# Optimization experiments

Hardware: AMD Instinct MI355X
Metric: run time of the kernel (lower is better)

## Reference

```python
import jax, jax.numpy as jnp
import numpy as np

B, T, H, D = 256, 128, 256, 256
N_SUB = 2  # fixed-step RK4 substeps per observation interval (replaces adaptive odeint)


def setup_inputs() -> dict:
    key = jax.random.key(0)
    ks = jax.random.split(key, 16)
    # timestamps: strictly increasing, shared across batch (torch code uses b[0,:,0])
    times = jnp.cumsum(jax.random.uniform(ks[0], (T,), minval=0.05, maxval=0.15)) + 0.1
    vals = jax.random.uniform(ks[1], (B, T))
    b = jnp.stack([jnp.broadcast_to(times, (B, T)), vals], axis=-1)  # (B,T,2)
    u = jax.random.uniform(ks[2], (B, T))
    train_m = (u < 0.4).astype(jnp.float32)
    test_m = ((u >= 0.4) & (u < 0.7)).astype(jnp.float32)
    m = train_m + test_m  # disjoint -> in {0,1}
    h0 = jnp.zeros((B, H), jnp.float32)
    s = 0.05
    p = lambda k, shp: jax.random.normal(k, shp, jnp.float32) * s
    return {
        'b': b, 'm': m, 'train_m': train_m, 'test_m': test_m, 'h0': h0,
        # ODE func: Linear(H->D) then Linear(D->H) then tanh
        'W1': p(ks[3], (D, H)), 'b1': p(ks[4], (D,)),
        'W2': p(ks[5], (H, D)), 'b2': p(ks[6], (H,)),
        # GRUCell(input_size=1, hidden=H), torch layout (3H, in)
        'W_ih': p(ks[7], (3 * H, 1)), 'W_hh': p(ks[8], (3 * H, H)),
        'b_ih': p(ks[9], (3 * H,)), 'b_hh': p(ks[10], (3 * H,)),
        # output heads: Linear(H->D), Linear(D->1), tanh
        'Wo1': p(ks[11], (D, H)), 'bo1': p(ks[12], (D,)),
        'Wo2': p(ks[13], (1, D)), 'bo2': p(ks[14], (1,)),
    }


def _gru(x, h, W_ih, W_hh, b_ih, b_hh):
    gi = x @ W_ih.T + b_ih          # (B, 3H)
    gh = h @ W_hh.T + b_hh          # (B, 3H)
    i_r, i_z, i_n = jnp.split(gi, 3, axis=-1)
    h_r, h_z, h_n = jnp.split(gh, 3, axis=-1)
    r = jax.nn.sigmoid(i_r + h_r)
    z = jax.nn.sigmoid(i_z + h_z)
    n = jnp.tanh(i_n + r * h_n)
    return (1.0 - z) * n + z * h


def _ode_rnn(b, m, train_m, test_m, h0, W1, b1, W2, b2,
             W_ih, W_hh, b_ih, b_hh, Wo1, bo1, Wo2, bo2):
    f = lambda x: jnp.tanh((x @ W1.T + b1) @ W2.T + b2)  # autonomous ODE func

    def rk4(h, t0, t1):
        dt = (t1 - t0) / N_SUB
        def sub(h, _):
            k1 = f(h)
            k2 = f(h + 0.5 * dt * k1)
            k3 = f(h + 0.5 * dt * k2)
            k4 = f(h + dt * k3)
            return h + (dt / 6.0) * (k1 + 2.0 * k2 + 2.0 * k3 + k4), None
        h, _ = jax.lax.scan(sub, h, None, length=N_SUB)
        return h

    times = b[0, :, 0]                                      # (T,)
    t0s = jnp.concatenate([jnp.zeros((1,), times.dtype), times[:-1]])
    vals = b[:, :, 1]                                       # (B,T)

    def step(h, inp):
        t0, t1, bv, mv, trm, tem = inp
        hp = rk4(h, t0, t1)                                 # (B,H)
        out = jnp.tanh((hp @ Wo1.T + bo1) @ Wo2.T + bo2)[:, 0]  # (B,)
        htrain = _gru((bv * trm)[:, None], hp, W_ih, W_hh, b_ih, b_hh)
        htest = _gru((out * tem)[:, None], hp, W_ih, W_hh, b_ih, b_hh)
        h_new = trm[:, None] * htrain + tem[:, None] * htest + (1.0 - mv)[:, None] * hp
        return h_new, out

    xs = (t0s, times, vals.T, m.T, train_m.T, test_m.T)
    _, outs = jax.lax.scan(step, h0, xs)                    # outs: (T,B)
    return outs.T                                           # (B,T)


def reference(b, m, train_m, test_m, h0, W1, b1, W2, b2,
              W_ih, W_hh, b_ih, b_hh, Wo1, bo1, Wo2, bo2):
    return _ode_rnn(b, m, train_m, test_m, h0, W1, b1, W2, b2,
                    W_ih, W_hh, b_ih, b_hh, Wo1, bo1, Wo2, bo2)
```

## Files before the change

kernel.cpp:

```cpp
#include <hip/hip_runtime.h>

#define H 256
#define T_STEPS 128
#define B_BATCH 256
#define I_LDS 48
#define XGRP 36

#define LOG2E 1.4426950408889634f

__device__ __forceinline__ float fexp2_(float x) {
#if __has_builtin(__builtin_amdgcn_exp2f)
    return __builtin_amdgcn_exp2f(x);
#else
    return exp2f(x);
#endif
}
__device__ __forceinline__ float frcp_(float x) {
#if __has_builtin(__builtin_amdgcn_rcpf)
    float r = __builtin_amdgcn_rcpf(x);
    return r * (2.0f - x * r);
#else
    return 1.0f / x;
#endif
}
__device__ __forceinline__ float tanhf_(float x) {
    float xc = fminf(fmaxf(x, -16.f), 16.f);
    float t  = fexp2_(xc * (2.f * LOG2E));
    return (t - 1.f) * frcp_(t + 1.f);
}
__device__ __forceinline__ float sigmoidf_(float x) {
    float xc = fminf(fmaxf(x, -30.f), 30.f);
    return frcp_(1.f + fexp2_(-xc * LOG2E));
}


__global__ void prep_weff(const float* __restrict__ W1, const float* __restrict__ W2,
                          const float* __restrict__ b1, const float* __restrict__ b2,
                          float* __restrict__ Weff, float* __restrict__ beff) {
    int i = blockIdx.x, j = threadIdx.x;
    const float* w2row = W2 + j * H;
    float acc = 0.f;
    for (int d = 0; d < H; ++d) acc += W1[d * H + i] * w2row[d];
    Weff[i * H + j] = acc;
    if (i == 0) {
        float bacc = b2[j];
        for (int d = 0; d < H; ++d) bacc += b1[d] * w2row[d];
        beff[j] = bacc;
    }
}

__global__ void prep_whht(const float* __restrict__ Whh, float* __restrict__ WhhT) {
    int idx = blockIdx.x * blockDim.x + threadIdx.x;
    int i = idx / 768;
    int r = idx - i * 768;
    WhhT[idx] = Whh[r * H + i];
}

__global__ void prep_wo(const float* __restrict__ Wo1, const float* __restrict__ Wo2,
                        const float* __restrict__ bo1, const float* __restrict__ bo2,
                        float* __restrict__ wo, float* __restrict__ bo) {
    int i = threadIdx.x;
    float acc = 0.f;
    for (int d = 0; d < H; ++d) acc += Wo1[d * H + i] * Wo2[d];
    wo[i] = acc;
    float p = bo1[i] * Wo2[i];
    __shared__ float red[4];
    for (int off = 32; off > 0; off >>= 1) p += __shfl_down(p, off);
    if ((i & 63) == 0) red[i >> 6] = p;
    __syncthreads();
    if (i == 0) bo[0] = red[0] + red[1] + red[2] + red[3] + bo2[0];
}


__global__ __attribute__((amdgpu_flat_work_group_size(1024, 1024),
                          amdgpu_waves_per_eu(4, 4)))
void ode_rnn_main(
    const float* __restrict__ b_in, const float* __restrict__ m_in,
    const float* __restrict__ trm_in, const float* __restrict__ tem_in,
    const float* __restrict__ h0,
    const float* __restrict__ Weff, const float* __restrict__ beff,
    const float* __restrict__ WhhT,
    const float* __restrict__ W_ih, const float* __restrict__ b_ih,
    const float* __restrict__ b_hh,
    const float* __restrict__ wo, const float* __restrict__ bo_p,
    float* __restrict__ out)
{
    const int tid = threadIdx.x;
    const int bb  = blockIdx.x;
    const int jp  = tid >> 3;
    const int e   = tid & 7;
    const int c   = e & 1;
    const int jc  = 2 * jp + c;

    __shared__ float whh_lds[I_LDS * 768];
    __shared__ __align__(16) float xsb[2][8 * XGRP];
    __shared__ __align__(16) float xsf[H];
    __shared__ float gh_lds[768];
    __shared__ float red[4];
    __shared__ float times_s[T_STEPS];
    __shared__ float bv_s[T_STEPS], trm_s[T_STEPS], tem_s[T_STEPS], m_s[T_STEPS];

    float2 wregv[32];
    #pragma unroll
    for (int il = 0; il < 32; ++il)
        wregv[il] = *(const float2*)&Weff[(32 * e + il) * H + 2 * jp];
    #pragma unroll
    for (int il = 0; il < 32; ++il)
        asm volatile("" : "+v"(wregv[il].x), "+v"(wregv[il].y));

    for (int k = tid; k < I_LDS * 768; k += 1024) whh_lds[k] = WhhT[k];
    if (tid < T_STEPS) {
        times_s[tid] = b_in[2 * tid];
        int bt = bb * T_STEPS + tid;
        bv_s[tid]  = b_in[2 * bt + 1];
        trm_s[tid] = trm_in[bt];
        tem_s[tid] = tem_in[bt];
        m_s[tid]   = m_in[bt];
    }

    float h = h0[bb * H + jc];
    const float be   = beff[jc];
    const float bihr = b_ih[jc], bihz = b_ih[H + jc], bihn = b_ih[2 * H + jc];
    const float bhhr = b_hh[jc], bhhz = b_hh[H + jc], bhhn = b_hh[2 * H + jc];
    const float wihr = W_ih[jc], wihz = W_ih[H + jc], wihn = W_ih[2 * H + jc];
    const float bo   = bo_p[0];
    const float wo_t = (tid >= 768) ? wo[tid - 768] : 0.f;

    const int pubpos = (jc >> 5) * XGRP + (jc & 31);

    if (e < 2) xsb[0][pubpos] = h;
    __syncthreads();

    #define EVAL(KOUT_) do {                                       \
        const float* xp_ = &xsb[cur][e * XGRP];                    \
        float a0_ = 0.f, a1_ = 0.f, b0_ = 0.f, b1_ = 0.f;          \
        _Pragma("unroll")                                          \
        for (int g_ = 0; g_ < 8; ++g_) {                           \
            float4 x_ = ((const float4*)xp_)[g_];                  \
            a0_ = fmaf(x_.x, wregv[4 * g_ + 0].x, a0_);            \
            b0_ = fmaf(x_.x, wregv[4 * g_ + 0].y, b0_);            \
            a1_ = fmaf(x_.y, wregv[4 * g_ + 1].x, a1_);            \
            b1_ = fmaf(x_.y, wregv[4 * g_ + 1].y, b1_);            \
            a0_ = fmaf(x_.z, wregv[4 * g_ + 2].x, a0_);            \
            b0_ = fmaf(x_.z, wregv[4 * g_ + 2].y, b0_);            \
            a1_ = fmaf(x_.w, wregv[4 * g_ + 3].x, a1_);            \
            b1_ = fmaf(x_.w, wregv[4 * g_ + 3].y, b1_);            \
        }                                                          \
        float s0_ = a0_ + a1_, s1_ = b0_ + b1_;                    \
        float v_ = (c == 0) ? s0_ : s1_;                           \
        float u_ = (c == 0) ? s1_ : s0_;                           \
        v_ += __shfl_xor(u_, 1);                                   \
        v_ += __shfl_xor(v_, 2);                                   \
        v_ += __shfl_xor(v_, 4);                                   \
        KOUT_ = tanhf_(be + v_);                                   \
    } while (0)

    #define PUBLISH(V_) do {                                       \
        if (e < 2) xsb[cur ^ 1][pubpos] = (V_);                    \
        __syncthreads();                                           \
        cur ^= 1;                                                  \
    } while (0)

    float tprev = 0.f;
    #pragma unroll 1
    for (int t = 0; t < T_STEPS; ++t) {
        float t1 = times_s[t];
        float dt = (t1 - tprev) * 0.5f;
        tprev = t1;

        int cur = 0;
        float k1, k2, k3, k4;
        #pragma unroll 1
        for (int s = 0; s < 2; ++s) {
            EVAL(k1); PUBLISH(fmaf(0.5f * dt, k1, h));
            EVAL(k2); PUBLISH(fmaf(0.5f * dt, k2, h));
            EVAL(k3); PUBLISH(fmaf(dt, k3, h));
            EVAL(k4);
            h = fmaf(dt * (1.f / 6.f), k1 + 2.f * (k2 + k3) + k4, h);
            if (s == 0) PUBLISH(h);
        }

        if (e < 2) xsf[jc] = h;
        __syncthreads();

        if (tid < 768) {
            float g0 = 0.f, g1 = 0.f, g2 = 0.f, g3 = 0.f;
            const float* wl = whh_lds + tid;
            #pragma unroll 4
            for (int i = 0; i < I_LDS; i += 4) {
                float4 xv = *(const float4*)(xsf + i);
                g0 = fmaf(xv.x, wl[(i + 0) * 768], g0);
                g1 = fmaf(xv.y, wl[(i + 1) * 768], g1);
                g2 = fmaf(xv.z, wl[(i + 2) * 768], g2);
                g3 = fmaf(xv.w, wl[(i + 3) * 768], g3);
            }
            const float* wr = WhhT + I_LDS * 768 + tid;
            #pragma unroll 8
            for (int i = 0; i < H - I_LDS; i += 4) {
                float4 xv = *(const float4*)(xsf + I_LDS + i);
                g0 = fmaf(xv.x, wr[(i + 0) * 768], g0);
                g1 = fmaf(xv.y, wr[(i + 1) * 768], g1);
                g2 = fmaf(xv.z, wr[(i + 2) * 768], g2);
                g3 = fmaf(xv.w, wr[(i + 3) * 768], g3);
            }
            gh_lds[tid] = (g0 + g1) + (g2 + g3);
        } else {
            float p = xsf[tid - 768] * wo_t;
            #pragma unroll
            for (int off = 32; off > 0; off >>= 1) p += __shfl_down(p, off);
            if ((tid & 63) == 0) red[(tid - 768) >> 6] = p;
        }
        __syncthreads();

        {
            float outv = tanhf_(red[0] + red[1] + red[2] + red[3] + bo);
            float bv = bv_s[t], trm = trm_s[t], tem = tem_s[t], mv = m_s[t];
            float ghr = gh_lds[jc] + bhhr;
            float ghz = gh_lds[256 + jc] + bhhz;
            float ghn = gh_lds[512 + jc] + bhhn;
            float x1v = bv * trm, x2v = outv * tem;

            float r1 = sigmoidf_(fmaf(x1v, wihr, bihr) + ghr);
            float z1 = sigmoidf_(fmaf(x1v, wihz, bihz) + ghz);
            float n1 = tanhf_(fmaf(x1v, wihn, bihn) + r1 * ghn);
            float h1 = (1.f - z1) * n1 + z1 * h;

            float r2 = sigmoidf_(fmaf(x2v, wihr, bihr) + ghr);
            float z2 = sigmoidf_(fmaf(x2v, wihz, bihz) + ghz);
            float n2 = tanhf_(fmaf(x2v, wihn, bihn) + r2 * ghn);
            float h2 = (1.f - z2) * n2 + z2 * h;

            if (tid == 0) out[bb * T_STEPS + t] = outv;
            h = trm * h1 + tem * h2 + (1.f - mv) * h;
        }

        if (e < 2) xsb[0][pubpos] = h;
        __syncthreads();
    }
    #undef EVAL
    #undef PUBLISH
}


extern "C" void kernel_launch(void* const* d_in, const int* in_sizes, int n_in,
                              void* d_out, int out_size, void* d_ws, size_t ws_size,
                              hipStream_t stream) {
    const float* b_in = (const float*)d_in[0];
    const float* m_in = (const float*)d_in[1];
    const float* trm  = (const float*)d_in[2];
    const float* tem  = (const float*)d_in[3];
    const float* h0   = (const float*)d_in[4];
    const float* W1   = (const float*)d_in[5];
    const float* b1   = (const float*)d_in[6];
    const float* W2   = (const float*)d_in[7];
    const float* b2   = (const float*)d_in[8];
    const float* W_ih = (const float*)d_in[9];
    const float* W_hh = (const float*)d_in[10];
    const float* b_ih = (const float*)d_in[11];
    const float* b_hh = (const float*)d_in[12];
    const float* Wo1  = (const float*)d_in[13];
    const float* bo1  = (const float*)d_in[14];
    const float* Wo2  = (const float*)d_in[15];
    const float* bo2  = (const float*)d_in[16];

    float* ws   = (float*)d_ws;
    float* Weff = ws;
    float* beff = Weff + 65536;
    float* WhhT = beff + 256;
    float* wo   = WhhT + 196608;
    float* bo   = wo + 256;

    prep_weff<<<256, 256, 0, stream>>>(W1, W2, b1, b2, Weff, beff);
    prep_whht<<<192, 1024, 0, stream>>>(W_hh, WhhT);
    prep_wo<<<1, 256, 0, stream>>>(Wo1, Wo2, bo1, bo2, wo, bo);

    ode_rnn_main<<<B_BATCH, 1024, 0, stream>>>(b_in, m_in, trm, tem, h0,
                                               Weff, beff, WhhT,
                                               W_ih, b_ih, b_hh, wo, bo,
                                               (float*)d_out);
}
```

Measured before the change: 2.024 ms.

## Keep GRU hidden weights in registers and split the matvec across quads

```diff
diff --git a/kernel.cpp b/kernel.cpp
--- a/kernel.cpp
+++ b/kernel.cpp
@@ -3,8 +3,8 @@
 #define H 256
 #define T_STEPS 128
 #define B_BATCH 256
-#define I_LDS 48
 #define XGRP 36
+#define X2STR 72
 
 #define LOG2E 1.4426950408889634f
 
@@ -91,12 +91,13 @@
     const int e   = tid & 7;
     const int c   = e & 1;
     const int jc  = 2 * jp + c;
-
-    __shared__ float whh_lds[I_LDS * 768];
+    const int o   = tid >> 2;
+    const int q   = tid & 3;
+
     __shared__ __align__(16) float xsb[2][8 * XGRP];
-    __shared__ __align__(16) float xsf[H];
+    __shared__ __align__(16) float xsf2[4 * X2STR];
     __shared__ float gh_lds[768];
-    __shared__ float red[4];
+    __shared__ float ohead[16];
     __shared__ float times_s[T_STEPS];
     __shared__ float bv_s[T_STEPS], trm_s[T_STEPS], tem_s[T_STEPS], m_s[T_STEPS];
 
@@ -108,7 +109,20 @@
     for (int il = 0; il < 32; ++il)
         asm volatile("" : "+v"(wregv[il].x), "+v"(wregv[il].y));
 
-    for (int k = tid; k < I_LDS * 768; k += 1024) whh_lds[k] = WhhT[k];
+    float wregh0[64], wregh1[64], wregh2[64];
+    {
+        const float* wb = WhhT + (64 * q) * 768 + o;
+        #pragma unroll
+        for (int i = 0; i < 64; ++i) {
+            wregh0[i] = wb[i * 768];
+            wregh1[i] = wb[i * 768 + 256];
+            wregh2[i] = wb[i * 768 + 512];
+        }
+    }
+    #pragma unroll
+    for (int i = 0; i < 64; ++i)
+        asm volatile("" : "+v"(wregh0[i]), "+v"(wregh1[i]), "+v"(wregh2[i]));
+
     if (tid < T_STEPS) {
         times_s[tid] = b_in[2 * tid];
         int bt = bb * T_STEPS + tid;
@@ -124,7 +138,7 @@
     const float bhhr = b_hh[jc], bhhz = b_hh[H + jc], bhhn = b_hh[2 * H + jc];
     const float wihr = W_ih[jc], wihz = W_ih[H + jc], wihn = W_ih[2 * H + jc];
     const float bo   = bo_p[0];
-    const float wo_t = (tid >= 768) ? wo[tid - 768] : 0.f;
+    const float wo_o = wo[o];
 
     const int pubpos = (jc >> 5) * XGRP + (jc & 31);
 
@@ -180,40 +194,47 @@
             if (s == 0) PUBLISH(h);
         }
 
-        if (e < 2) xsf[jc] = h;
+        if (e < 2) xsf2[jc + 8 * (jc >> 6)] = h;
         __syncthreads();
 
-        if (tid < 768) {
-            float g0 = 0.f, g1 = 0.f, g2 = 0.f, g3 = 0.f;
-            const float* wl = whh_lds + tid;
-            #pragma unroll 4
-            for (int i = 0; i < I_LDS; i += 4) {
-                float4 xv = *(const float4*)(xsf + i);
-                g0 = fmaf(xv.x, wl[(i + 0) * 768], g0);
-                g1 = fmaf(xv.y, wl[(i + 1) * 768], g1);
-                g2 = fmaf(xv.z, wl[(i + 2) * 768], g2);
-                g3 = fmaf(xv.w, wl[(i + 3) * 768], g3);
+        {
+            const float* xb = &xsf2[X2STR * q];
+            float pg0 = 0.f, pg1 = 0.f, pg2 = 0.f;
+            #pragma unroll
+            for (int ii = 0; ii < 16; ++ii) {
+                float4 x = *(const float4*)(xb + 4 * ii);
+                pg0 = fmaf(x.x, wregh0[4 * ii + 0], pg0);
+                pg1 = fmaf(x.x, wregh1[4 * ii + 0], pg1);
+                pg2 = fmaf(x.x, wregh2[4 * ii + 0], pg2);
+                pg0 = fmaf(x.y, wregh0[4 * ii + 1], pg0);
+                pg1 = fmaf(x.y, wregh1[4 * ii + 1], pg1);
+                pg2 = fmaf(x.y, wregh2[4 * ii + 1], pg2);
+                pg0 = fmaf(x.z, wregh0[4 * ii + 2], pg0);
+                pg1 = fmaf(x.z, wregh1[4 * ii + 2], pg1);
+                pg2 = fmaf(x.z, wregh2[4 * ii + 2], pg2);
+                pg0 = fmaf(x.w, wregh0[4 * ii + 3], pg0);
+                pg1 = fmaf(x.w, wregh1[4 * ii + 3], pg1);
+                pg2 = fmaf(x.w, wregh2[4 * ii + 3], pg2);
             }
-            const float* wr = WhhT + I_LDS * 768 + tid;
-            #pragma unroll 8
-            for (int i = 0; i < H - I_LDS; i += 4) {
-                float4 xv = *(const float4*)(xsf + I_LDS + i);
-                g0 = fmaf(xv.x, wr[(i + 0) * 768], g0);
-                g1 = fmaf(xv.y, wr[(i + 1) * 768], g1);
-                g2 = fmaf(xv.z, wr[(i + 2) * 768], g2);
-                g3 = fmaf(xv.w, wr[(i + 3) * 768], g3);
-            }
-            gh_lds[tid] = (g0 + g1) + (g2 + g3);
-        } else {
-            float p = xsf[tid - 768] * wo_t;
-            #pragma unroll
-            for (int off = 32; off > 0; off >>= 1) p += __shfl_down(p, off);
-            if ((tid & 63) == 0) red[(tid - 768) >> 6] = p;
+            pg0 += __shfl_xor(pg0, 1); pg0 += __shfl_xor(pg0, 2);
+            pg1 += __shfl_xor(pg1, 1); pg1 += __shfl_xor(pg1, 2);
+            pg2 += __shfl_xor(pg2, 1); pg2 += __shfl_xor(pg2, 2);
+            float pgsel = (q == 0) ? pg0 : (q == 1) ? pg1 : pg2;
+            if (q < 3) gh_lds[q * 256 + o] = pgsel;
+
+            float ph = xsf2[o + 8 * (o >> 6)] * wo_o;
+            ph += __shfl_xor(ph, 1);  ph += __shfl_xor(ph, 2);
+            ph += __shfl_xor(ph, 4);  ph += __shfl_xor(ph, 8);
+            ph += __shfl_xor(ph, 16); ph += __shfl_xor(ph, 32);
+            if ((tid & 63) == 0) ohead[tid >> 6] = ph * 0.25f;
         }
         __syncthreads();
 
         {
-            float outv = tanhf_(red[0] + red[1] + red[2] + red[3] + bo);
+            float osum = 0.f;
+            #pragma unroll
+            for (int w = 0; w < 16; ++w) osum += ohead[w];
+            float outv = tanhf_(osum + bo);
             float bv = bv_s[t], trm = trm_s[t], tem = tem_s[t], mv = m_s[t];
             float ghr = gh_lds[jc] + bhhr;
             float ghz = gh_lds[256 + jc] + bhhz;
```

New measurement: 7.747 ms. +282.7%, slower.
